# Kernel tuning notes

Measured on AMD Instinct MI355X. Metric: run time of the kernel, lower is better.

## Reference

```python
import jax, jax.numpy as jnp
import numpy as np

B, N, K, D = 2, 4096, 20, 128
PH = 8          # pos_mlp hidden dim
AH = 4 * D      # attn_mlp hidden dim (attn_mlp_hidden_mult=4)


def setup_inputs() -> dict:
    key = jax.random.key(0)
    ks = jax.random.split(key, 12)
    s = 0.02
    f32 = jnp.float32
    return {
        "x": jax.random.normal(ks[0], (B, N, 3), f32),
        "pos": jax.random.normal(ks[1], (B, N, 3), f32),
        # linear1/2/3 (torch Linear: y = x @ W.T + b)
        "W1": jax.random.normal(ks[2], (D, 3), f32) * s,  "b1": jnp.zeros((D,), f32),
        "W2": jax.random.normal(ks[3], (D, D), f32) * s,  "b2": jnp.zeros((D,), f32),
        "W3": jax.random.normal(ks[4], (D, D), f32) * s,  "b3": jnp.zeros((D,), f32),
        # PointTransformerLayer params
        "Wqkv": jax.random.normal(ks[5], (3 * D, D), f32) * s,          # to_qkv, no bias
        "Wp1": jax.random.normal(ks[6], (PH, 3), f32) * s,  "bp1": jnp.zeros((PH,), f32),
        "Wp2": jax.random.normal(ks[7], (D, PH), f32) * s,  "bp2": jnp.zeros((D,), f32),
        "Wa1": jax.random.normal(ks[8], (AH, D), f32) * s,  "ba1": jnp.zeros((AH,), f32),
        "Wa2": jax.random.normal(ks[9], (D, AH), f32) * s,  "ba2": jnp.zeros((D,), f32),
    }


def reference(x, pos, W1, b1, W2, b2, W3, b3, Wqkv,
              Wp1, bp1, Wp2, bp2, Wa1, ba1, Wa2, ba2):
    h = x @ W1.T + b1            # [B,N,D] linear1
    h1 = h @ W2.T + b2           # [B,N,D] linear2

    # --- PointTransformerLayer (lucidrains, KNN vector attention) ---
    qkv = h1 @ Wqkv.T            # [B,N,3D]
    q, k, v = jnp.split(qkv, 3, axis=-1)

    # squared pairwise distances and K nearest neighbors (self included)
    d2 = jnp.sum((pos[:, :, None, :] - pos[:, None, :, :]) ** 2, axis=-1)  # [B,N,N]
    _, idx = jax.lax.top_k(-d2, K)                                          # [B,N,K]

    gather = jax.vmap(lambda arr, ind: arr[ind])  # per-batch gather -> [B,N,K,*]
    kn = gather(k, idx)          # [B,N,K,D]
    vn = gather(v, idx)          # [B,N,K,D]
    pn = gather(pos, idx)        # [B,N,K,3]

    rel = pos[:, :, None, :] - pn                                   # [B,N,K,3]
    pe = jax.nn.relu(rel @ Wp1.T + bp1) @ Wp2.T + bp2               # pos_mlp [B,N,K,D]

    vn = vn + pe
    sim = jax.nn.relu((q[:, :, None, :] - kn + pe) @ Wa1.T + ba1) @ Wa2.T + ba2  # attn_mlp
    attn = jax.nn.softmax(sim, axis=2)                              # softmax over neighbors
    agg = jnp.sum(attn * vn, axis=2)                                # [B,N,D]

    return h + (agg @ W3.T + b3)  # residual: x + linear3(x1)
```

## Files before the change

### kernel.cpp

```cpp
#include <hip/hip_runtime.h>
#include <stdint.h>

#define BB 2
#define NN 4096
#define KNB 20
#define DD 128
#define PHH 8
#define AHH 512
#define BN (BB*NN)

typedef unsigned short ushort_t;
typedef short bf16x8 __attribute__((ext_vector_type(8)));
typedef float f32x4 __attribute__((ext_vector_type(4)));

__device__ __forceinline__ uint32_t umin32(uint32_t a, uint32_t b) { return a < b ? a : b; }
__device__ __forceinline__ uint32_t umax32(uint32_t a, uint32_t b) { return a > b ? a : b; }

__device__ __forceinline__ float bf2f(ushort_t u) {
    union { float f; uint32_t i; } c; c.i = ((uint32_t)u) << 16; return c.f;
}
__device__ __forceinline__ uint32_t cvt_pk_bf16(float lo, float hi) {
    uint32_t r;
    asm("v_cvt_pk_bf16_f32 %0, %1, %2" : "=v"(r) : "v"(lo), "v"(hi));
    return r;
}
__device__ __forceinline__ ushort_t f2bf(float f) {
    return (ushort_t)(cvt_pk_bf16(f, f) & 0xFFFFu);
}
__device__ __forceinline__ bf16x8 load_bfrag(const float* __restrict__ src) {
    float4 x = *(const float4*)src;
    float4 y = *(const float4*)(src + 4);
    union { bf16x8 v; uint32_t u[4]; } r;
    r.u[0] = cvt_pk_bf16(x.x, x.y);
    r.u[1] = cvt_pk_bf16(x.z, x.w);
    r.u[2] = cvt_pk_bf16(y.x, y.y);
    r.u[3] = cvt_pk_bf16(y.z, y.w);
    return r.v;
}

#define SW256(m, byteInRow) ((m)*256 + ((byteInRow) ^ (((m)&7) << 4)))

__global__ __launch_bounds__(256) void k_prep(
        const float* __restrict__ Wa1f, const float* __restrict__ Wa2f,
        const float* __restrict__ Wp2f, const float* __restrict__ pos,
        ushort_t* __restrict__ Wa1bf, ushort_t* __restrict__ Wa2bf,
        ushort_t* __restrict__ Wfusebf, float* __restrict__ psoa) {
    int bid = blockIdx.x, tid = threadIdx.x;
    if (bid < 64) {
        int base = bid * 2048 + tid * 8;
        const float* src = (base < 65536) ? (Wa1f + base) : (Wa2f + (base - 65536));
        ushort_t* dst = (base < 65536) ? (Wa1bf + base) : (Wa2bf + (base - 65536));
        union { ushort_t u[8]; uint4 q; } pk;
        #pragma unroll
        for (int i = 0; i < 8; ++i) pk.u[i] = f2bf(src[i]);
        *(uint4*)dst = pk.q;
    } else if (bid < 66) {
        int a = (bid - 64) * 256 + tid;
        float s[PHH];
        #pragma unroll
        for (int jj = 0; jj < PHH; ++jj) s[jj] = 0.f;
        for (int d = 0; d < DD; ++d) {
            float wv = Wa1f[(size_t)a*DD + d];
            #pragma unroll
            for (int jj = 0; jj < PHH; ++jj) s[jj] += wv * Wp2f[d*PHH + jj];
        }
        union { ushort_t u[8]; uint4 q; } pk;
        #pragma unroll
        for (int jj = 0; jj < PHH; ++jj) pk.u[jj] = f2bf(s[jj]);
        *(uint4*)&Wfusebf[a*PHH] = pk.q;
    } else {
        int e0 = (bid - 66) * 2048 + tid * 8;
        float v[8];
        #pragma unroll
        for (int i = 0; i < 8; ++i) {
            int el = e0 + i;
            int comp = el >> 13;
            int rem = el & 8191;
            v[i] = pos[(size_t)rem*3 + comp];
        }
        #pragma unroll
        for (int i = 0; i < 8; i += 4)
            *(float4*)&psoa[e0 + i] = (float4){v[i], v[i+1], v[i+2], v[i+3]};
    }
}

__global__ __launch_bounds__(256) void k_front(
        const float* __restrict__ x,
        const float* __restrict__ W1, const float* __restrict__ b1,
        const float* __restrict__ W2f, const float* __restrict__ b2,
        const float* __restrict__ Wqkvf,
        const ushort_t* __restrict__ Wa1bf, const float* __restrict__ ba1,
        float* __restrict__ h, ushort_t* __restrict__ vf,
        ushort_t* __restrict__ QWbf, ushort_t* __restrict__ KWbf) {
    __shared__ __align__(16) char smem[16896];
    float* xs = (float*)(smem + 16384);
    int tid = threadIdx.x, w = tid >> 6, lane = tid & 63;
    int lg = lane >> 4, c16 = lane & 15;
    int p0 = blockIdx.x * 32;

    if (tid < 96) xs[tid] = x[(size_t)p0*3 + tid];
    __syncthreads();

    #pragma unroll
    for (int it = 0; it < 16; ++it) {
        int lin = it*256 + tid;
        int m = lin >> 7, d = lin & 127;
        float hv = b1[d] + xs[m*3+0]*W1[d*3+0] + xs[m*3+1]*W1[d*3+1] + xs[m*3+2]*W1[d*3+2];
        h[(size_t)(p0+m)*DD + d] = hv;
        *(ushort_t*)&smem[SW256(m, d*2)] = f2bf(hv);
    }
    __syncthreads();

    {
        f32x4 acc[2][2];
        #pragma unroll
        for (int mt = 0; mt < 2; ++mt)
            #pragma unroll
            for (int ntl = 0; ntl < 2; ++ntl) acc[mt][ntl] = (f32x4){0,0,0,0};
        #pragma unroll
        for (int ks = 0; ks < 4; ++ks) {
            int k0 = ks*32 + lg*8;
            bf16x8 aF[2];
            #pragma unroll
            for (int mt = 0; mt < 2; ++mt)
                aF[mt] = *(const bf16x8*)&smem[SW256(mt*16 + c16, k0*2)];
            #pragma unroll
            for (int ntl = 0; ntl < 2; ++ntl) {
                int n = (2*w + ntl)*16 + c16;
                bf16x8 bF = load_bfrag(W2f + (size_t)n*DD + k0);
                #pragma unroll
                for (int mt = 0; mt < 2; ++mt)
                    acc[mt][ntl] = __builtin_amdgcn_mfma_f32_16x16x32_bf16(aF[mt], bF, acc[mt][ntl], 0, 0, 0);
            }
        }
        #pragma unroll
        for (int ntl = 0; ntl < 2; ++ntl) {
            int n = (2*w + ntl)*16 + c16;
            float bias = b2[n];
            #pragma unroll
            for (int mt = 0; mt < 2; ++mt)
                #pragma unroll
                for (int i = 0; i < 4; ++i) {
                    int m = mt*16 + lg*4 + i;
                    *(ushort_t*)&smem[8192 + SW256(m, n*2)] = f2bf(acc[mt][ntl][i] + bias);
                }
        }
    }
    __syncthreads();

    {
        f32x4 acc[2][6];
        #pragma unroll
        for (int mt = 0; mt < 2; ++mt)
            #pragma unroll
            for (int ntl = 0; ntl < 6; ++ntl) acc[mt][ntl] = (f32x4){0,0,0,0};
        #pragma unroll
        for (int ks = 0; ks < 4; ++ks) {
            int k0 = ks*32 + lg*8;
            bf16x8 aF[2];
            #pragma unroll
            for (int mt = 0; mt < 2; ++mt)
                aF[mt] = *(const bf16x8*)&smem[8192 + SW256(mt*16 + c16, k0*2)];
            #pragma unroll
            for (int ntl = 0; ntl < 6; ++ntl) {
                int n = (w*6 + ntl)*16 + c16;
                bf16x8 bF = load_bfrag(Wqkvf + (size_t)n*DD + k0);
                #pragma unroll
                for (int mt = 0; mt < 2; ++mt)
                    acc[mt][ntl] = __builtin_amdgcn_mfma_f32_16x16x32_bf16(aF[mt], bF, acc[mt][ntl], 0, 0, 0);
            }
        }
        #pragma unroll
        for (int ntl = 0; ntl < 6; ++ntl) {
            int n = (w*6 + ntl)*16 + c16;
            int r = n >> 7, d = n & 127;
            #pragma unroll
            for (int mt = 0; mt < 2; ++mt)
                #pragma unroll
                for (int i = 0; i < 4; ++i) {
                    int m = mt*16 + lg*4 + i;
                    if (r == 0) *(ushort_t*)&smem[SW256(m, d*2)] = f2bf(acc[mt][ntl][i]);
                    else if (r == 2) vf[(size_t)(p0+m)*DD + d] = f2bf(acc[mt][ntl][i]);
                }
        }
        __syncthreads();
        #pragma unroll
        for (int ntl = 0; ntl < 6; ++ntl) {
            int n = (w*6 + ntl)*16 + c16;
            int r = n >> 7, d = n & 127;
            if (r == 1) {
                #pragma unroll
                for (int mt = 0; mt < 2; ++mt)
                    #pragma unroll
                    for (int i = 0; i < 4; ++i) {
                        int m = mt*16 + lg*4 + i;
                        *(ushort_t*)&smem[8192 + SW256(m, d*2)] = f2bf(acc[mt][ntl][i]);
                    }
            }
        }
    }
    __syncthreads();

    #pragma unroll
    for (int half = 0; half < 2; ++half) {
        f32x4 accQ[2][4], accK[2][4];
        #pragma unroll
        for (int mt = 0; mt < 2; ++mt)
            #pragma unroll
            for (int ntl = 0; ntl < 4; ++ntl) {
                accQ[mt][ntl] = (f32x4){0,0,0,0};
                accK[mt][ntl] = (f32x4){0,0,0,0};
            }
        #pragma unroll
        for (int ks = 0; ks < 4; ++ks) {
            int k0 = ks*32 + lg*8;
            bf16x8 aQ[2], aK[2];
            #pragma unroll
            for (int mt = 0; mt < 2; ++mt) {
                aQ[mt] = *(const bf16x8*)&smem[SW256(mt*16 + c16, k0*2)];
                aK[mt] = *(const bf16x8*)&smem[8192 + SW256(mt*16 + c16, k0*2)];
            }
            #pragma unroll
            for (int ntl = 0; ntl < 4; ++ntl) {
                int n = (w*8 + half*4 + ntl)*16 + c16;
                bf16x8 bF = *(const bf16x8*)&Wa1bf[(size_t)n*DD + k0];
                #pragma unroll
                for (int mt = 0; mt < 2; ++mt) {
                    accQ[mt][ntl] = __builtin_amdgcn_mfma_f32_16x16x32_bf16(aQ[mt], bF, accQ[mt][ntl], 0, 0, 0);
                    accK[mt][ntl] = __builtin_amdgcn_mfma_f32_16x16x32_bf16(aK[mt], bF, accK[mt][ntl], 0, 0, 0);
                }
            }
        }
        #pragma unroll
        for (int ntl = 0; ntl < 4; ++ntl) {
            int n = (w*8 + half*4 + ntl)*16 + c16;
            float bias = ba1[n];
            #pragma unroll
            for (int mt = 0; mt < 2; ++mt)
                #pragma unroll
                for (int i = 0; i < 4; ++i) {
                    int m = mt*16 + lg*4 + i;
                    QWbf[(size_t)(p0+m)*AHH + n] = f2bf(accQ[mt][ntl][i] + bias);
                    KWbf[(size_t)(p0+m)*AHH + n] = f2bf(accK[mt][ntl][i]);
                }
        }
    }
}

__global__ __launch_bounds__(256) void k_knn(const float* __restrict__ pos,
                                             const float* __restrict__ psoa,
                                             int* __restrict__ idx) {
    int wid  = threadIdx.x >> 6;
    int lane = threadIdx.x & 63;
    int p = blockIdx.x*4 + wid;
    int b = p >> 12;
    float qx = pos[p*3+0], qy = pos[p*3+1], qz = pos[p*3+2];
    const float4* px4 = (const float4*)(psoa + (size_t)b*NN);
    const float4* py4 = (const float4*)(psoa + 8192 + (size_t)b*NN);
    const float4* pz4 = (const float4*)(psoa + 16384 + (size_t)b*NN);

    uint32_t bk[KNB];
    #pragma unroll
    for (int i = 0; i < KNB; ++i) bk[i] = 0xFFFFFFFFu;

    for (int it = 0; it < NN/256; ++it) {
        int j4 = it*64 + lane;
        float4 X = px4[j4], Y = py4[j4], Z = pz4[j4];
        #pragma unroll
        for (int c = 0; c < 4; ++c) {
            float dx = qx - ((c==0)?X.x:(c==1)?X.y:(c==2)?X.z:X.w);
            float dy = qy - ((c==0)?Y.x:(c==1)?Y.y:(c==2)?Y.z:Y.w);
            float dz = qz - ((c==0)?Z.x:(c==1)?Z.y:(c==2)?Z.z:Z.w);
            float d2 = dx*dx + dy*dy + dz*dz;
            uint32_t key = (__float_as_uint(d2) & 0xFFFFF000u) | (uint32_t)(j4*4 + c);
            if (key < bk[KNB-1]) {
                uint32_t cc = key;
                #pragma unroll
                for (int t = 0; t < KNB; ++t) {
                    uint32_t lo = umin32(cc, bk[t]);
                    uint32_t hi = umax32(cc, bk[t]);
                    bk[t] = lo; cc = hi;
                }
            }
        }
    }
    for (int r = 0; r < KNB; ++r) {
        uint32_t m = bk[0];
        #pragma unroll
        for (int s = 1; s < 64; s <<= 1)
            m = umin32(m, (uint32_t)__shfl_xor((int)m, s, 64));
        if (lane == 0) idx[(size_t)p*KNB + r] = (int)(m & 0xFFFu);
        bool win = (bk[0] == m);
        #pragma unroll
        for (int t = 0; t < KNB-1; ++t) bk[t] = win ? bk[t+1] : bk[t];
        bk[KNB-1] = win ? 0xFFFFFFFFu : bk[KNB-1];
    }
}

#define TL_OFF 0
#define PH_OFF 20480
#define NIDX_OFF 21760

__global__ __launch_bounds__(256, 4) void k_attn(
        const float* __restrict__ pos,
        const ushort_t* __restrict__ QWbf, const ushort_t* __restrict__ KWbf,
        const ushort_t* __restrict__ vf, const int* __restrict__ idx,
        const float* __restrict__ Wp1, const float* __restrict__ bp1,
        const float* __restrict__ Wp2, const float* __restrict__ bp2,
        const ushort_t* __restrict__ Wfusebf,
        const ushort_t* __restrict__ Wa2bf, const float* __restrict__ ba2,
        float* __restrict__ agg) {
    __shared__ __align__(16) char smem[22080];
    int* nidx = (int*)(smem + NIDX_OFF);

    int tid = threadIdx.x, w = tid >> 6, lane = tid & 63;
    int lg = lane >> 4, c16 = lane & 15;
    int bid = blockIdx.x;
    int xcd = bid & 7, sloc = bid >> 3;
    int b = xcd >> 2;
    int p0 = b*NN + ((xcd & 3)*256 + sloc)*4;

    if (tid < 80) nidx[tid] = idx[(size_t)(p0 + tid/20)*KNB + (tid%20)];
    __syncthreads();

    if (tid < 80) {
        int m = tid, g = m / 20;
        int j = nidx[m];
        const float* pq = pos + (size_t)(p0+g)*3;
        const float* pn = pos + (size_t)(b*NN+j)*3;
        float r0 = pq[0]-pn[0], r1 = pq[1]-pn[1], r2 = pq[2]-pn[2];
        union { ushort_t u[8]; uint4 q; } pk;
        #pragma unroll
        for (int jj = 0; jj < PHH; ++jj) {
            float a = bp1[jj] + r0*Wp1[jj*3+0] + r1*Wp1[jj*3+1] + r2*Wp1[jj*3+2];
            pk.u[jj] = f2bf(fmaxf(a, 0.f));
        }
        *(uint4*)&smem[PH_OFF + m*16] = pk.q;
    }
    __syncthreads();

    int dA = w*32 + 2*c16, dB = dA + 1;
    float bp2A = bp2[dA], bp2B = bp2[dB];
    float ba2A = ba2[dA], ba2B = ba2[dB];

    bf16x8 bP0 = {0,0,0,0,0,0,0,0}, bP1 = {0,0,0,0,0,0,0,0};
    if (lg == 0) {
        bP0 = load_bfrag(Wp2 + (size_t)dA*PHH);
        bP1 = load_bfrag(Wp2 + (size_t)dB*PHH);
    }
    uint32_t vpe_pk[5][4];
    #pragma unroll
    for (int mt = 0; mt < 5; ++mt) {
        bf16x8 aP = {0,0,0,0,0,0,0,0};
        if (lg == 0) aP = *(const bf16x8*)&smem[PH_OFF + (mt*16 + c16)*16];
        f32x4 accP0 = (f32x4){0,0,0,0}, accP1 = (f32x4){0,0,0,0};
        accP0 = __builtin_amdgcn_mfma_f32_16x16x32_bf16(aP, bP0, accP0, 0, 0, 0);
        accP1 = __builtin_amdgcn_mfma_f32_16x16x32_bf16(aP, bP1, accP1, 0, 0, 0);
        #pragma unroll
        for (int i = 0; i < 4; ++i) {
            int m = mt*16 + lg*4 + i;
            int j = nidx[m];
            uint32_t vw = *(const uint32_t*)&vf[(size_t)(b*NN+j)*DD + dA];
            float peA = accP0[i] + bp2A;
            float peB = accP1[i] + bp2B;
            vpe_pk[mt][i] = cvt_pk_bf16(bf2f((ushort_t)(vw & 0xFFFFu)) + peA,
                                        bf2f((ushort_t)(vw >> 16)) + peB);
        }
    }

    f32x4 accS[5][2];
    #pragma unroll
    for (int mt = 0; mt < 5; ++mt)
        #pragma unroll
        for (int ntl = 0; ntl < 2; ++ntl) accS[mt][ntl] = (f32x4){0,0,0,0};

    for (int c = 0; c < 4; ++c) {
        int aQ0 = c*128 + dA;
        bf16x8 bF0 = {0,0,0,0,0,0,0,0}, bF1 = {0,0,0,0,0,0,0,0};
        if (lg == 0) {
            bF0 = *(const bf16x8*)&Wfusebf[(size_t)aQ0*PHH];
            bF1 = *(const bf16x8*)&Wfusebf[(size_t)(aQ0+1)*PHH];
        }
        uint32_t qww[4];
        #pragma unroll
        for (int g = 0; g < 4; ++g)
            qww[g] = *(const uint32_t*)&QWbf[(size_t)(p0+g)*AHH + aQ0];
        uint32_t kwn[4];
        #pragma unroll
        for (int i = 0; i < 4; ++i)
            kwn[i] = *(const uint32_t*)&KWbf[(size_t)(b*NN + nidx[lg*4 + i])*AHH + aQ0];
        #pragma unroll
        for (int mt = 0; mt < 5; ++mt) {
            uint32_t kwc[4];
            #pragma unroll
            for (int i = 0; i < 4; ++i) kwc[i] = kwn[i];
            if (mt < 4) {
                #pragma unroll
                for (int i = 0; i < 4; ++i)
                    kwn[i] = *(const uint32_t*)&KWbf[(size_t)(b*NN + nidx[(mt+1)*16 + lg*4 + i])*AHH + aQ0];
            }
            bf16x8 aP = {0,0,0,0,0,0,0,0};
            if (lg == 0) aP = *(const bf16x8*)&smem[PH_OFF + (mt*16 + c16)*16];
            f32x4 accF0 = (f32x4){0,0,0,0}, accF1 = (f32x4){0,0,0,0};
            accF0 = __builtin_amdgcn_mfma_f32_16x16x32_bf16(aP, bF0, accF0, 0, 0, 0);
            accF1 = __builtin_amdgcn_mfma_f32_16x16x32_bf16(aP, bF1, accF1, 0, 0, 0);
            uint32_t qsel = (mt==0) ? qww[0]
                          : (mt==1) ? (lg>=1 ? qww[1] : qww[0])
                          : (mt==2) ? (lg>=2 ? qww[2] : qww[1])
                          : (mt==3) ? (lg==3 ? qww[3] : qww[2])
                          : qww[3];
            float qA = bf2f((ushort_t)(qsel & 0xFFFFu));
            float qB = bf2f((ushort_t)(qsel >> 16));
            #pragma unroll
            for (int i = 0; i < 4; ++i) {
                int m = mt*16 + lg*4 + i;
                float kA = bf2f((ushort_t)(kwc[i] & 0xFFFFu));
                float kB = bf2f((ushort_t)(kwc[i] >> 16));
                float tA = fmaxf(qA - kA + accF0[i], 0.f);
                float tB = fmaxf(qB - kB + accF1[i], 0.f);
                *(uint32_t*)&smem[TL_OFF + SW256(m, dA*2)] = cvt_pk_bf16(tA, tB);
            }
        }
        __syncthreads();

        __builtin_amdgcn_s_setprio(1);
        #pragma unroll
        for (int ks = 0; ks < 4; ++ks) {
            int k0 = ks*32 + lg*8;
            bf16x8 aF[5];
            #pragma unroll
            for (int mt = 0; mt < 5; ++mt)
                aF[mt] = *(const bf16x8*)&smem[TL_OFF + SW256(mt*16 + c16, k0*2)];
            bf16x8 bW0 = *(const bf16x8*)&Wa2bf[(size_t)dA*AHH + c*128 + k0];
            bf16x8 bW1 = *(const bf16x8*)&Wa2bf[(size_t)dB*AHH + c*128 + k0];
            #pragma unroll
            for (int mt = 0; mt < 5; ++mt) {
                accS[mt][0] = __builtin_amdgcn_mfma_f32_16x16x32_bf16(aF[mt], bW0, accS[mt][0], 0, 0, 0);
                accS[mt][1] = __builtin_amdgcn_mfma_f32_16x16x32_bf16(aF[mt], bW1, accS[mt][1], 0, 0, 0);
            }
        }
        __builtin_amdgcn_s_setprio(0);
        __syncthreads();
    }

    float s_mtA[5], a_mtA[5], s_mtB[5], a_mtB[5];
    #pragma unroll
    for (int mt = 0; mt < 5; ++mt) {
        float sa = 0.f, aa = 0.f, sb = 0.f, ab = 0.f;
        #pragma unroll
        for (int i = 0; i < 4; ++i) {
            float eA = __expf(accS[mt][0][i] + ba2A);
            float eB = __expf(accS[mt][1][i] + ba2B);
            uint32_t pk = vpe_pk[mt][i];
            float vA = bf2f((ushort_t)(pk & 0xFFFFu));
            float vB = bf2f((ushort_t)(pk >> 16));
            sa += eA; aa += eA*vA;
            sb += eB; ab += eB*vB;
        }
        s_mtA[mt] = sa; a_mtA[mt] = aa; s_mtB[mt] = sb; a_mtB[mt] = ab;
    }
    bool eq0 = (lg==0), ge1 = (lg>=1), ge2 = (lg>=2), le1 = (lg<=1), le2 = (lg<=2), eq3 = (lg==3);
    float s0A = s_mtA[0] + (eq0 ? s_mtA[1] : 0.f);
    float s1A = (ge1 ? s_mtA[1] : 0.f) + (le1 ? s_mtA[2] : 0.f);
    float s2A = (ge2 ? s_mtA[2] : 0.f) + (le2 ? s_mtA[3] : 0.f);
    float s3A = (eq3 ? s_mtA[3] : 0.f) + s_mtA[4];
    float a0A = a_mtA[0] + (eq0 ? a_mtA[1] : 0.f);
    float a1A = (ge1 ? a_mtA[1] : 0.f) + (le1 ? a_mtA[2] : 0.f);
    float a2A = (ge2 ? a_mtA[2] : 0.f) + (le2 ? a_mtA[3] : 0.f);
    float a3A = (eq3 ? a_mtA[3] : 0.f) + a_mtA[4];
    float s0B = s_mtB[0] + (eq0 ? s_mtB[1] : 0.f);
    float s1B = (ge1 ? s_mtB[1] : 0.f) + (le1 ? s_mtB[2] : 0.f);
    float s2B = (ge2 ? s_mtB[2] : 0.f) + (le2 ? s_mtB[3] : 0.f);
    float s3B = (eq3 ? s_mtB[3] : 0.f) + s_mtB[4];
    float a0B = a_mtB[0] + (eq0 ? a_mtB[1] : 0.f);
    float a1B = (ge1 ? a_mtB[1] : 0.f) + (le1 ? a_mtB[2] : 0.f);
    float a2B = (ge2 ? a_mtB[2] : 0.f) + (le2 ? a_mtB[3] : 0.f);
    float a3B = (eq3 ? a_mtB[3] : 0.f) + a_mtB[4];

    #define RED2(v) { v += __shfl_xor(v, 16, 64); v += __shfl_xor(v, 32, 64); }
    RED2(s0A) RED2(s1A) RED2(s2A) RED2(s3A)
    RED2(a0A) RED2(a1A) RED2(a2A) RED2(a3A)
    RED2(s0B) RED2(s1B) RED2(s2B) RED2(s3B)
    RED2(a0B) RED2(a1B) RED2(a2B) RED2(a3B)
    #undef RED2

    float myS_A = (lg==0) ? s0A : (lg==1) ? s1A : (lg==2) ? s2A : s3A;
    float myA_A = (lg==0) ? a0A : (lg==1) ? a1A : (lg==2) ? a2A : a3A;
    float myS_B = (lg==0) ? s0B : (lg==1) ? s1B : (lg==2) ? s2B : s3B;
    float myA_B = (lg==0) ? a0B : (lg==1) ? a1B : (lg==2) ? a2B : a3B;
    float2 st;
    st.x = myA_A / myS_A;
    st.y = myA_B / myS_B;
    *(float2*)&agg[(size_t)(p0+lg)*DD + dA] = st;
}

__global__ __launch_bounds__(256) void k_out(
        const float* __restrict__ agg, const float* __restrict__ h,
        const float* __restrict__ W3f, const float* __restrict__ b3,
        float* __restrict__ out) {
    __shared__ __align__(16) char smem[8192];
    int tid = threadIdx.x, w = tid >> 6, lane = tid & 63;
    int p0 = blockIdx.x * 32;

    #pragma unroll
    for (int it = 0; it < 16; ++it) {
        int lin = it*256 + tid;
        int m = lin >> 7, d = lin & 127;
        *(ushort_t*)&smem[SW256(m, d*2)] = f2bf(agg[(size_t)(p0+m)*DD + d]);
    }
    __syncthreads();

    f32x4 acc[2][2];
    #pragma unroll
    for (int mt = 0; mt < 2; ++mt)
        #pragma unroll
        for (int ntl = 0; ntl < 2; ++ntl) acc[mt][ntl] = (f32x4){0,0,0,0};
    #pragma unroll
    for (int ks = 0; ks < 4; ++ks) {
        int k0 = ks*32 + (lane >> 4)*8;
        bf16x8 aF[2];
        #pragma unroll
        for (int mt = 0; mt < 2; ++mt)
            aF[mt] = *(const bf16x8*)&smem[SW256(mt*16 + (lane & 15), k0*2)];
        #pragma unroll
        for (int ntl = 0; ntl < 2; ++ntl) {
            int n = (2*w + ntl)*16 + (lane & 15);
            bf16x8 bF = load_bfrag(W3f + (size_t)n*DD + k0);
            #pragma unroll
            for (int mt = 0; mt < 2; ++mt)
                acc[mt][ntl] = __builtin_amdgcn_mfma_f32_16x16x32_bf16(aF[mt], bF, acc[mt][ntl], 0, 0, 0);
        }
    }
    #pragma unroll
    for (int ntl = 0; ntl < 2; ++ntl) {
        int n = (2*w + ntl)*16 + (lane & 15);
        float bias = b3[n];
        #pragma unroll
        for (int mt = 0; mt < 2; ++mt)
            #pragma unroll
            for (int i = 0; i < 4; ++i) {
                int m = mt*16 + (lane >> 4)*4 + i;
                size_t o = (size_t)(p0+m)*DD + n;
                out[o] = acc[mt][ntl][i] + bias + h[o];
            }
    }
}

extern "C" void kernel_launch(void* const* d_in, const int* in_sizes, int n_in,
                              void* d_out, int out_size, void* d_ws, size_t ws_size,
                              hipStream_t stream) {
    const float* x    = (const float*)d_in[0];
    const float* pos  = (const float*)d_in[1];
    const float* W1   = (const float*)d_in[2];
    const float* b1   = (const float*)d_in[3];
    const float* W2   = (const float*)d_in[4];
    const float* b2   = (const float*)d_in[5];
    const float* W3   = (const float*)d_in[6];
    const float* b3   = (const float*)d_in[7];
    const float* Wqkv = (const float*)d_in[8];
    const float* Wp1  = (const float*)d_in[9];
    const float* bp1  = (const float*)d_in[10];
    const float* Wp2  = (const float*)d_in[11];
    const float* bp2  = (const float*)d_in[12];
    const float* Wa1  = (const float*)d_in[13];
    const float* ba1  = (const float*)d_in[14];
    const float* Wa2  = (const float*)d_in[15];
    const float* ba2  = (const float*)d_in[16];

    char* W = (char*)d_ws;
    float*    h       = (float*)(W + 0);
    float*    agg     = (float*)(W + 4194304);
    ushort_t* vf      = (ushort_t*)(W + 8388608);
    ushort_t* QWbf    = (ushort_t*)(W + 10485760);
    ushort_t* KWbf    = (ushort_t*)(W + 18874368);
    int*      idx     = (int*)(W + 27262976);
    ushort_t* Wa1bf   = (ushort_t*)(W + 27918336);
    ushort_t* Wa2bf   = (ushort_t*)(W + 28049408);
    ushort_t* Wfusebf = (ushort_t*)(W + 28180480);
    float*    psoa    = (float*)(W + 28188672);

    k_prep <<<78, 256, 0, stream>>>(Wa1, Wa2, Wp2, pos, Wa1bf, Wa2bf, Wfusebf, psoa);
    k_front<<<BN/32, 256, 0, stream>>>(x, W1, b1, W2, b2, Wqkv, Wa1bf, ba1,
                                       h, vf, QWbf, KWbf);
    k_knn  <<<BN/4, 256, 0, stream>>>(pos, psoa, idx);
    k_attn <<<BN/4, 256, 0, stream>>>(pos, QWbf, KWbf, vf, idx,
                                      Wp1, bp1, Wp2, bp2, Wfusebf, Wa2bf, ba2, agg);
    k_out  <<<BN/32, 256, 0, stream>>>(agg, h, W3, b3, (float*)d_out);
}
```

Measured before the change: 163.5 us.

## Halve rows per block in front/out kernels and batch neighbor gathers in attention

```diff
diff --git a/kernel.cpp b/kernel.cpp
--- a/kernel.cpp
+++ b/kernel.cpp
@@ -96,13 +96,13 @@
     float* xs = (float*)(smem + 16384);
     int tid = threadIdx.x, w = tid >> 6, lane = tid & 63;
     int lg = lane >> 4, c16 = lane & 15;
-    int p0 = blockIdx.x * 32;
-
-    if (tid < 96) xs[tid] = x[(size_t)p0*3 + tid];
-    __syncthreads();
-
-    #pragma unroll
-    for (int it = 0; it < 16; ++it) {
+    int p0 = blockIdx.x * 16;
+
+    if (tid < 48) xs[tid] = x[(size_t)p0*3 + tid];
+    __syncthreads();
+
+    #pragma unroll
+    for (int it = 0; it < 8; ++it) {
         int lin = it*256 + tid;
         int m = lin >> 7, d = lin & 127;
         float hv = b1[d] + xs[m*3+0]*W1[d*3+0] + xs[m*3+1]*W1[d*3+1] + xs[m*3+2]*W1[d*3+2];
@@ -112,25 +112,17 @@
     __syncthreads();
 
     {
-        f32x4 acc[2][2];
-        #pragma unroll
-        for (int mt = 0; mt < 2; ++mt)
-            #pragma unroll
-            for (int ntl = 0; ntl < 2; ++ntl) acc[mt][ntl] = (f32x4){0,0,0,0};
+        f32x4 acc[2];
+        acc[0] = (f32x4){0,0,0,0}; acc[1] = (f32x4){0,0,0,0};
         #pragma unroll
         for (int ks = 0; ks < 4; ++ks) {
             int k0 = ks*32 + lg*8;
-            bf16x8 aF[2];
-            #pragma unroll
-            for (int mt = 0; mt < 2; ++mt)
-                aF[mt] = *(const bf16x8*)&smem[SW256(mt*16 + c16, k0*2)];
+            bf16x8 aF = *(const bf16x8*)&smem[SW256(c16, k0*2)];
             #pragma unroll
             for (int ntl = 0; ntl < 2; ++ntl) {
                 int n = (2*w + ntl)*16 + c16;
                 bf16x8 bF = load_bfrag(W2f + (size_t)n*DD + k0);
-                #pragma unroll
-                for (int mt = 0; mt < 2; ++mt)
-                    acc[mt][ntl] = __builtin_amdgcn_mfma_f32_16x16x32_bf16(aF[mt], bF, acc[mt][ntl], 0, 0, 0);
+                acc[ntl] = __builtin_amdgcn_mfma_f32_16x16x32_bf16(aF, bF, acc[ntl], 0, 0, 0);
             }
         }
         #pragma unroll
@@ -138,36 +130,27 @@
             int n = (2*w + ntl)*16 + c16;
             float bias = b2[n];
             #pragma unroll
-            for (int mt = 0; mt < 2; ++mt)
-                #pragma unroll
-                for (int i = 0; i < 4; ++i) {
-                    int m = mt*16 + lg*4 + i;
-                    *(ushort_t*)&smem[8192 + SW256(m, n*2)] = f2bf(acc[mt][ntl][i] + bias);
-                }
+            for (int i = 0; i < 4; ++i) {
+                int m = lg*4 + i;
+                *(ushort_t*)&smem[8192 + SW256(m, n*2)] = f2bf(acc[ntl][i] + bias);
+            }
         }
     }
     __syncthreads();
 
     {
-        f32x4 acc[2][6];
-        #pragma unroll
-        for (int mt = 0; mt < 2; ++mt)
-            #pragma unroll
-            for (int ntl = 0; ntl < 6; ++ntl) acc[mt][ntl] = (f32x4){0,0,0,0};
+        f32x4 acc[6];
+        #pragma unroll
+        for (int ntl = 0; ntl < 6; ++ntl) acc[ntl] = (f32x4){0,0,0,0};
         #pragma unroll
         for (int ks = 0; ks < 4; ++ks) {
             int k0 = ks*32 + lg*8;
-            bf16x8 aF[2];
-            #pragma unroll
-            for (int mt = 0; mt < 2; ++mt)
-                aF[mt] = *(const bf16x8*)&smem[8192 + SW256(mt*16 + c16, k0*2)];
+            bf16x8 aF = *(const bf16x8*)&smem[8192 + SW256(c16, k0*2)];
             #pragma unroll
             for (int ntl = 0; ntl < 6; ++ntl) {
                 int n = (w*6 + ntl)*16 + c16;
                 bf16x8 bF = load_bfrag(Wqkvf + (size_t)n*DD + k0);
-                #pragma unroll
-                for (int mt = 0; mt < 2; ++mt)
-                    acc[mt][ntl] = __builtin_amdgcn_mfma_f32_16x16x32_bf16(aF[mt], bF, acc[mt][ntl], 0, 0, 0);
+                acc[ntl] = __builtin_amdgcn_mfma_f32_16x16x32_bf16(aF, bF, acc[ntl], 0, 0, 0);
             }
         }
         #pragma unroll
@@ -175,13 +158,11 @@
             int n = (w*6 + ntl)*16 + c16;
             int r = n >> 7, d = n & 127;
             #pragma unroll
-            for (int mt = 0; mt < 2; ++mt)
-                #pragma unroll
-                for (int i = 0; i < 4; ++i) {
-                    int m = mt*16 + lg*4 + i;
-                    if (r == 0) *(ushort_t*)&smem[SW256(m, d*2)] = f2bf(acc[mt][ntl][i]);
-                    else if (r == 2) vf[(size_t)(p0+m)*DD + d] = f2bf(acc[mt][ntl][i]);
-                }
+            for (int i = 0; i < 4; ++i) {
+                int m = lg*4 + i;
+                if (r == 0) *(ushort_t*)&smem[SW256(m, d*2)] = f2bf(acc[ntl][i]);
+                else if (r == 2) vf[(size_t)(p0+m)*DD + d] = f2bf(acc[ntl][i]);
+            }
         }
         __syncthreads();
         #pragma unroll
@@ -190,12 +171,10 @@
             int r = n >> 7, d = n & 127;
             if (r == 1) {
                 #pragma unroll
-                for (int mt = 0; mt < 2; ++mt)
-                    #pragma unroll
-                    for (int i = 0; i < 4; ++i) {
-                        int m = mt*16 + lg*4 + i;
-                        *(ushort_t*)&smem[8192 + SW256(m, d*2)] = f2bf(acc[mt][ntl][i]);
-                    }
+                for (int i = 0; i < 4; ++i) {
+                    int m = lg*4 + i;
+                    *(ushort_t*)&smem[8192 + SW256(m, d*2)] = f2bf(acc[ntl][i]);
+                }
             }
         }
     }
@@ -203,32 +182,23 @@
 
     #pragma unroll
     for (int half = 0; half < 2; ++half) {
-        f32x4 accQ[2][4], accK[2][4];
-        #pragma unroll
-        for (int mt = 0; mt < 2; ++mt)
-            #pragma unroll
-            for (int ntl = 0; ntl < 4; ++ntl) {
-                accQ[mt][ntl] = (f32x4){0,0,0,0};
-                accK[mt][ntl] = (f32x4){0,0,0,0};
-            }
+        f32x4 accQ[4], accK[4];
+        #pragma unroll
+        for (int ntl = 0; ntl < 4; ++ntl) {
+            accQ[ntl] = (f32x4){0,0,0,0};
+            accK[ntl] = (f32x4){0,0,0,0};
+        }
         #pragma unroll
         for (int ks = 0; ks < 4; ++ks) {
             int k0 = ks*32 + lg*8;
-            bf16x8 aQ[2], aK[2];
-            #pragma unroll
-            for (int mt = 0; mt < 2; ++mt) {
-                aQ[mt] = *(const bf16x8*)&smem[SW256(mt*16 + c16, k0*2)];
-                aK[mt] = *(const bf16x8*)&smem[8192 + SW256(mt*16 + c16, k0*2)];
-            }
+            bf16x8 aQ = *(const bf16x8*)&smem[SW256(c16, k0*2)];
+            bf16x8 aK = *(const bf16x8*)&smem[8192 + SW256(c16, k0*2)];
             #pragma unroll
             for (int ntl = 0; ntl < 4; ++ntl) {
                 int n = (w*8 + half*4 + ntl)*16 + c16;
                 bf16x8 bF = *(const bf16x8*)&Wa1bf[(size_t)n*DD + k0];
-                #pragma unroll
-                for (int mt = 0; mt < 2; ++mt) {
-                    accQ[mt][ntl] = __builtin_amdgcn_mfma_f32_16x16x32_bf16(aQ[mt], bF, accQ[mt][ntl], 0, 0, 0);
-                    accK[mt][ntl] = __builtin_amdgcn_mfma_f32_16x16x32_bf16(aK[mt], bF, accK[mt][ntl], 0, 0, 0);
-                }
+                accQ[ntl] = __builtin_amdgcn_mfma_f32_16x16x32_bf16(aQ, bF, accQ[ntl], 0, 0, 0);
+                accK[ntl] = __builtin_amdgcn_mfma_f32_16x16x32_bf16(aK, bF, accK[ntl], 0, 0, 0);
             }
         }
         #pragma unroll
@@ -236,13 +206,11 @@
             int n = (w*8 + half*4 + ntl)*16 + c16;
             float bias = ba1[n];
             #pragma unroll
-            for (int mt = 0; mt < 2; ++mt)
-                #pragma unroll
-                for (int i = 0; i < 4; ++i) {
-                    int m = mt*16 + lg*4 + i;
-                    QWbf[(size_t)(p0+m)*AHH + n] = f2bf(accQ[mt][ntl][i] + bias);
-                    KWbf[(size_t)(p0+m)*AHH + n] = f2bf(accK[mt][ntl][i]);
-                }
+            for (int i = 0; i < 4; ++i) {
+                int m = lg*4 + i;
+                QWbf[(size_t)(p0+m)*AHH + n] = f2bf(accQ[ntl][i] + bias);
+                KWbf[(size_t)(p0+m)*AHH + n] = f2bf(accK[ntl][i]);
+            }
         }
     }
 }
@@ -348,6 +316,14 @@
         bP0 = load_bfrag(Wp2 + (size_t)dA*PHH);
         bP1 = load_bfrag(Wp2 + (size_t)dB*PHH);
     }
+    uint32_t vw[5][4];
+    #pragma unroll
+    for (int mt = 0; mt < 5; ++mt)
+        #pragma unroll
+        for (int i = 0; i < 4; ++i) {
+            int j = nidx[mt*16 + lg*4 + i];
+            vw[mt][i] = *(const uint32_t*)&vf[(size_t)(b*NN+j)*DD + dA];
+        }
     uint32_t vpe_pk[5][4];
     #pragma unroll
     for (int mt = 0; mt < 5; ++mt) {
@@ -358,13 +334,10 @@
         accP1 = __builtin_amdgcn_mfma_f32_16x16x32_bf16(aP, bP1, accP1, 0, 0, 0);
         #pragma unroll
         for (int i = 0; i < 4; ++i) {
-            int m = mt*16 + lg*4 + i;
-            int j = nidx[m];
-            uint32_t vw = *(const uint32_t*)&vf[(size_t)(b*NN+j)*DD + dA];
             float peA = accP0[i] + bp2A;
             float peB = accP1[i] + bp2B;
-            vpe_pk[mt][i] = cvt_pk_bf16(bf2f((ushort_t)(vw & 0xFFFFu)) + peA,
-                                        bf2f((ushort_t)(vw >> 16)) + peB);
+            vpe_pk[mt][i] = cvt_pk_bf16(bf2f((ushort_t)(vw[mt][i] & 0xFFFFu)) + peA,
+                                        bf2f((ushort_t)(vw[mt][i] >> 16)) + peB);
         }
     }
 
@@ -376,29 +349,22 @@
 
     for (int c = 0; c < 4; ++c) {
         int aQ0 = c*128 + dA;
+        uint32_t qww[4], kww[5][4];
+        #pragma unroll
+        for (int g = 0; g < 4; ++g)
+            qww[g] = *(const uint32_t*)&QWbf[(size_t)(p0+g)*AHH + aQ0];
+        #pragma unroll
+        for (int mt = 0; mt < 5; ++mt)
+            #pragma unroll
+            for (int i = 0; i < 4; ++i)
+                kww[mt][i] = *(const uint32_t*)&KWbf[(size_t)(b*NN + nidx[mt*16 + lg*4 + i])*AHH + aQ0];
         bf16x8 bF0 = {0,0,0,0,0,0,0,0}, bF1 = {0,0,0,0,0,0,0,0};
         if (lg == 0) {
             bF0 = *(const bf16x8*)&Wfusebf[(size_t)aQ0*PHH];
             bF1 = *(const bf16x8*)&Wfusebf[(size_t)(aQ0+1)*PHH];
         }
-        uint32_t qww[4];
-        #pragma unroll
-        for (int g = 0; g < 4; ++g)
-            qww[g] = *(const uint32_t*)&QWbf[(size_t)(p0+g)*AHH + aQ0];
-        uint32_t kwn[4];
-        #pragma unroll
-        for (int i = 0; i < 4; ++i)
-            kwn[i] = *(const uint32_t*)&KWbf[(size_t)(b*NN + nidx[lg*4 + i])*AHH + aQ0];
         #pragma unroll
         for (int mt = 0; mt < 5; ++mt) {
-            uint32_t kwc[4];
-            #pragma unroll
-            for (int i = 0; i < 4; ++i) kwc[i] = kwn[i];
-            if (mt < 4) {
-                #pragma unroll
-                for (int i = 0; i < 4; ++i)
-                    kwn[i] = *(const uint32_t*)&KWbf[(size_t)(b*NN + nidx[(mt+1)*16 + lg*4 + i])*AHH + aQ0];
-            }
             bf16x8 aP = {0,0,0,0,0,0,0,0};
             if (lg == 0) aP = *(const bf16x8*)&smem[PH_OFF + (mt*16 + c16)*16];
             f32x4 accF0 = (f32x4){0,0,0,0}, accF1 = (f32x4){0,0,0,0};
@@ -414,8 +380,8 @@
             #pragma unroll
             for (int i = 0; i < 4; ++i) {
                 int m = mt*16 + lg*4 + i;
-                float kA = bf2f((ushort_t)(kwc[i] & 0xFFFFu));
-                float kB = bf2f((ushort_t)(kwc[i] >> 16));
+                float kA = bf2f((ushort_t)(kww[mt][i] & 0xFFFFu));
+                float kB = bf2f((ushort_t)(kww[mt][i] >> 16));
                 float tA = fmaxf(qA - kA + accF0[i], 0.f);
                 float tB = fmaxf(qB - kB + accF1[i], 0.f);
                 *(uint32_t*)&smem[TL_OFF + SW256(m, dA*2)] = cvt_pk_bf16(tA, tB);
@@ -498,51 +464,42 @@
         const float* __restrict__ agg, const float* __restrict__ h,
         const float* __restrict__ W3f, const float* __restrict__ b3,
         float* __restrict__ out) {
-    __shared__ __align__(16) char smem[8192];
+    __shared__ __align__(16) char smem[4096];
     int tid = threadIdx.x, w = tid >> 6, lane = tid & 63;
-    int p0 = blockIdx.x * 32;
-
-    #pragma unroll
-    for (int it = 0; it < 16; ++it) {
+    int lg = lane >> 4, c16 = lane & 15;
+    int p0 = blockIdx.x * 16;
+
+    #pragma unroll
+    for (int it = 0; it < 8; ++it) {
         int lin = it*256 + tid;
         int m = lin >> 7, d = lin & 127;
         *(ushort_t*)&smem[SW256(m, d*2)] = f2bf(agg[(size_t)(p0+m)*DD + d]);
     }
     __syncthreads();
 
-    f32x4 acc[2][2];
-    #pragma unroll
-    for (int mt = 0; mt < 2; ++mt)
-        #pragma unroll
-        for (int ntl = 0; ntl < 2; ++ntl) acc[mt][ntl] = (f32x4){0,0,0,0};
+    f32x4 acc[2];
+    acc[0] = (f32x4){0,0,0,0}; acc[1] = (f32x4){0,0,0,0};
     #pragma unroll
     for (int ks = 0; ks < 4; ++ks) {
-        int k0 = ks*32 + (lane >> 4)*8;
-        bf16x8 aF[2];
-        #pragma unroll
-        for (int mt = 0; mt < 2; ++mt)
-            aF[mt] = *(const bf16x8*)&smem[SW256(mt*16 + (lane & 15), k0*2)];
+        int k0 = ks*32 + lg*8;
+        bf16x8 aF = *(const bf16x8*)&smem[SW256(c16, k0*2)];
         #pragma unroll
         for (int ntl = 0; ntl < 2; ++ntl) {
-            int n = (2*w + ntl)*16 + (lane & 15);
+            int n = (2*w + ntl)*16 + c16;
             bf16x8 bF = load_bfrag(W3f + (size_t)n*DD + k0);
-            #pragma unroll
-            for (int mt = 0; mt < 2; ++mt)
-                acc[mt][ntl] = __builtin_amdgcn_mfma_f32_16x16x32_bf16(aF[mt], bF, acc[mt][ntl], 0, 0, 0);
+            acc[ntl] = __builtin_amdgcn_mfma_f32_16x16x32_bf16(aF, bF, acc[ntl], 0, 0, 0);
         }
     }
     #pragma unroll
     for (int ntl = 0; ntl < 2; ++ntl) {
-        int n = (2*w + ntl)*16 + (lane & 15);
+        int n = (2*w + ntl)*16 + c16;
         float bias = b3[n];
         #pragma unroll
-        for (int mt = 0; mt < 2; ++mt)
-            #pragma unroll
-            for (int i = 0; i < 4; ++i) {
-                int m = mt*16 + (lane >> 4)*4 + i;
-                size_t o = (size_t)(p0+m)*DD + n;
-                out[o] = acc[mt][ntl][i] + bias + h[o];
-            }
+        for (int i = 0; i < 4; ++i) {
+            int m = lg*4 + i;
+            size_t o = (size_t)(p0+m)*DD + n;
+            out[o] = acc[ntl][i] + bias + h[o];
+        }
     }
 }
 
@@ -580,10 +537,10 @@
     float*    psoa    = (float*)(W + 28188672);
 
     k_prep <<<78, 256, 0, stream>>>(Wa1, Wa2, Wp2, pos, Wa1bf, Wa2bf, Wfusebf, psoa);
-    k_front<<<BN/32, 256, 0, stream>>>(x, W1, b1, W2, b2, Wqkv, Wa1bf, ba1,
+    k_front<<<BN/16, 256, 0, stream>>>(x, W1, b1, W2, b2, Wqkv, Wa1bf, ba1,
                                        h, vf, QWbf, KWbf);
     k_knn  <<<BN/4, 256, 0, stream>>>(pos, psoa, idx);
     k_attn <<<BN/4, 256, 0, stream>>>(pos, QWbf, KWbf, vf, idx,
                                       Wp1, bp1, Wp2, bp2, Wfusebf, Wa2bf, ba2, agg);
-    k_out  <<<BN/32, 256, 0, stream>>>(agg, h, W3, b3, (float*)d_out);
-}
+    k_out  <<<BN/16, 256, 0, stream>>>(agg, h, W3, b3, (float*)d_out);
+}
```

Measured after the change: 169.5 us. 1.04x slower.

## Fuse output projection and residual into attention kernel, pre-convert W3 to bf16

Applied to the files above, without the earlier changes.

```diff
diff --git a/kernel.cpp b/kernel.cpp
--- a/kernel.cpp
+++ b/kernel.cpp
@@ -42,9 +42,11 @@
 
 __global__ __launch_bounds__(256) void k_prep(
         const float* __restrict__ Wa1f, const float* __restrict__ Wa2f,
-        const float* __restrict__ Wp2f, const float* __restrict__ pos,
+        const float* __restrict__ W3f, const float* __restrict__ Wp2f,
+        const float* __restrict__ pos,
         ushort_t* __restrict__ Wa1bf, ushort_t* __restrict__ Wa2bf,
-        ushort_t* __restrict__ Wfusebf, float* __restrict__ psoa) {
+        ushort_t* __restrict__ W3bf, ushort_t* __restrict__ Wfusebf,
+        float* __restrict__ psoa) {
     int bid = blockIdx.x, tid = threadIdx.x;
     if (bid < 64) {
         int base = bid * 2048 + tid * 8;
@@ -54,8 +56,14 @@
         #pragma unroll
         for (int i = 0; i < 8; ++i) pk.u[i] = f2bf(src[i]);
         *(uint4*)dst = pk.q;
-    } else if (bid < 66) {
-        int a = (bid - 64) * 256 + tid;
+    } else if (bid < 72) {
+        int base = (bid - 64) * 2048 + tid * 8;
+        union { ushort_t u[8]; uint4 q; } pk;
+        #pragma unroll
+        for (int i = 0; i < 8; ++i) pk.u[i] = f2bf(W3f[base + i]);
+        *(uint4*)&W3bf[base] = pk.q;
+    } else if (bid < 74) {
+        int a = (bid - 72) * 256 + tid;
         float s[PHH];
         #pragma unroll
         for (int jj = 0; jj < PHH; ++jj) s[jj] = 0.f;
@@ -69,7 +77,7 @@
         for (int jj = 0; jj < PHH; ++jj) pk.u[jj] = f2bf(s[jj]);
         *(uint4*)&Wfusebf[a*PHH] = pk.q;
     } else {
-        int e0 = (bid - 66) * 2048 + tid * 8;
+        int e0 = (bid - 74) * 2048 + tid * 8;
         float v[8];
         #pragma unroll
         for (int i = 0; i < 8; ++i) {
@@ -309,7 +317,8 @@
         const float* __restrict__ Wp2, const float* __restrict__ bp2,
         const ushort_t* __restrict__ Wfusebf,
         const ushort_t* __restrict__ Wa2bf, const float* __restrict__ ba2,
-        float* __restrict__ agg) {
+        const ushort_t* __restrict__ W3bf, const float* __restrict__ b3,
+        const float* __restrict__ h, float* __restrict__ out) {
     __shared__ __align__(16) char smem[22080];
     int* nidx = (int*)(smem + NIDX_OFF);
 
@@ -488,61 +497,39 @@
     float myA_A = (lg==0) ? a0A : (lg==1) ? a1A : (lg==2) ? a2A : a3A;
     float myS_B = (lg==0) ? s0B : (lg==1) ? s1B : (lg==2) ? s2B : s3B;
     float myA_B = (lg==0) ? a0B : (lg==1) ? a1B : (lg==2) ? a2B : a3B;
-    float2 st;
-    st.x = myA_A / myS_A;
-    st.y = myA_B / myS_B;
-    *(float2*)&agg[(size_t)(p0+lg)*DD + dA] = st;
-}
-
-__global__ __launch_bounds__(256) void k_out(
-        const float* __restrict__ agg, const float* __restrict__ h,
-        const float* __restrict__ W3f, const float* __restrict__ b3,
-        float* __restrict__ out) {
-    __shared__ __align__(16) char smem[8192];
-    int tid = threadIdx.x, w = tid >> 6, lane = tid & 63;
-    int p0 = blockIdx.x * 32;
-
-    #pragma unroll
-    for (int it = 0; it < 16; ++it) {
-        int lin = it*256 + tid;
-        int m = lin >> 7, d = lin & 127;
-        *(ushort_t*)&smem[SW256(m, d*2)] = f2bf(agg[(size_t)(p0+m)*DD + d]);
-    }
-    __syncthreads();
-
-    f32x4 acc[2][2];
-    #pragma unroll
-    for (int mt = 0; mt < 2; ++mt)
-        #pragma unroll
-        for (int ntl = 0; ntl < 2; ++ntl) acc[mt][ntl] = (f32x4){0,0,0,0};
+    float aggA = myA_A / myS_A;
+    float aggB = myA_B / myS_B;
+
+    #pragma unroll
+    for (int z = 0; z < 3; ++z)
+        *(uint32_t*)&smem[TL_OFF + 1024 + (z*256 + tid)*4] = 0u;
+    *(uint32_t*)&smem[TL_OFF + SW256(lg, dA*2)] = cvt_pk_bf16(aggA, aggB);
+    __syncthreads();
+
+    f32x4 accO[2];
+    accO[0] = (f32x4){0,0,0,0}; accO[1] = (f32x4){0,0,0,0};
     #pragma unroll
     for (int ks = 0; ks < 4; ++ks) {
-        int k0 = ks*32 + (lane >> 4)*8;
-        bf16x8 aF[2];
-        #pragma unroll
-        for (int mt = 0; mt < 2; ++mt)
-            aF[mt] = *(const bf16x8*)&smem[SW256(mt*16 + (lane & 15), k0*2)];
+        int k0 = ks*32 + lg*8;
+        bf16x8 aF = *(const bf16x8*)&smem[TL_OFF + SW256(c16, k0*2)];
         #pragma unroll
         for (int ntl = 0; ntl < 2; ++ntl) {
-            int n = (2*w + ntl)*16 + (lane & 15);
-            bf16x8 bF = load_bfrag(W3f + (size_t)n*DD + k0);
-            #pragma unroll
-            for (int mt = 0; mt < 2; ++mt)
-                acc[mt][ntl] = __builtin_amdgcn_mfma_f32_16x16x32_bf16(aF[mt], bF, acc[mt][ntl], 0, 0, 0);
-        }
-    }
-    #pragma unroll
-    for (int ntl = 0; ntl < 2; ++ntl) {
-        int n = (2*w + ntl)*16 + (lane & 15);
-        float bias = b3[n];
-        #pragma unroll
-        for (int mt = 0; mt < 2; ++mt)
+            int n = (w*2 + ntl)*16 + c16;
+            bf16x8 bF = *(const bf16x8*)&W3bf[(size_t)n*DD + k0];
+            accO[ntl] = __builtin_amdgcn_mfma_f32_16x16x32_bf16(aF, bF, accO[ntl], 0, 0, 0);
+        }
+    }
+    if (lg == 0) {
+        #pragma unroll
+        for (int ntl = 0; ntl < 2; ++ntl) {
+            int n = (w*2 + ntl)*16 + c16;
+            float bias = b3[n];
             #pragma unroll
             for (int i = 0; i < 4; ++i) {
-                int m = mt*16 + (lane >> 4)*4 + i;
-                size_t o = (size_t)(p0+m)*DD + n;
-                out[o] = acc[mt][ntl][i] + bias + h[o];
-            }
+                size_t o = (size_t)(p0+i)*DD + n;
+                out[o] = accO[ntl][i] + bias + h[o];
+            }
+        }
     }
 }
 
@@ -569,7 +556,6 @@
 
     char* W = (char*)d_ws;
     float*    h       = (float*)(W + 0);
-    float*    agg     = (float*)(W + 4194304);
     ushort_t* vf      = (ushort_t*)(W + 8388608);
     ushort_t* QWbf    = (ushort_t*)(W + 10485760);
     ushort_t* KWbf    = (ushort_t*)(W + 18874368);
@@ -578,12 +564,14 @@
     ushort_t* Wa2bf   = (ushort_t*)(W + 28049408);
     ushort_t* Wfusebf = (ushort_t*)(W + 28180480);
     float*    psoa    = (float*)(W + 28188672);
-
-    k_prep <<<78, 256, 0, stream>>>(Wa1, Wa2, Wp2, pos, Wa1bf, Wa2bf, Wfusebf, psoa);
+    ushort_t* W3bf    = (ushort_t*)(W + 28286976);
+
+    k_prep <<<86, 256, 0, stream>>>(Wa1, Wa2, W3, Wp2, pos,
+                                    Wa1bf, Wa2bf, W3bf, Wfusebf, psoa);
     k_front<<<BN/32, 256, 0, stream>>>(x, W1, b1, W2, b2, Wqkv, Wa1bf, ba1,
                                        h, vf, QWbf, KWbf);
     k_knn  <<<BN/4, 256, 0, stream>>>(pos, psoa, idx);
     k_attn <<<BN/4, 256, 0, stream>>>(pos, QWbf, KWbf, vf, idx,
-                                      Wp1, bp1, Wp2, bp2, Wfusebf, Wa2bf, ba2, agg);
-    k_out  <<<BN/32, 256, 0, stream>>>(agg, h, W3, b3, (float*)d_out);
-}
+                                      Wp1, bp1, Wp2, bp2, Wfusebf, Wa2bf, ba2,
+                                      W3bf, b3, h, (float*)d_out);
+}
```

New measurement: 162.1 us, median of 2. Within noise of the previous version (-0.8%).
